# Kernel optimization log

Measured on AMD Instinct MI355X. Metric: run time of the kernel, lower is better.

## Reference

```python
import jax, jax.numpy as jnp
import numpy as np

D, H, W_IMG = 3, 128, 128
ZDIM, HDIM = 64, 512
KSEG, B = 8, 256
DIN = D * H * W_IMG


def setup_inputs() -> dict:
    key = jax.random.key(0)
    ks = jax.random.split(key, 18)
    s = 0.02
    inp = {
        "x": jax.random.normal(ks[0], (B, D, H, W_IMG), jnp.float32),
        "K": KSEG,
        "eps0": jax.random.normal(ks[1], (B, ZDIM), jnp.float32),
        "eps_q": jax.random.normal(ks[2], (KSEG - 1, B, ZDIM), jnp.float32),
        "eps_p": jax.random.normal(ks[3], (KSEG - 1, B, ZDIM), jnp.float32),
        # encoder stem (flattened image -> hdim) and gaussian head (hdim -> 2*zdim)
        "W_stem": jax.random.normal(ks[4], (DIN, HDIM), jnp.float32) * s,
        "b_stem": jnp.zeros((HDIM,), jnp.float32),
        "W_g": jax.random.normal(ks[5], (HDIM, 2 * ZDIM), jnp.float32) * s,
        "b_g": jnp.zeros((2 * ZDIM,), jnp.float32),
        # posterior LSTM (input zdim+hdim, hidden 2*zdim); initial state is always
        # zero in the original code (state is never fed back), so W_hh drops out.
        "Wih_q": jax.random.normal(ks[6], (ZDIM + HDIM, 8 * ZDIM), jnp.float32) * s,
        "b_q": jnp.zeros((8 * ZDIM,), jnp.float32),
        "Wlin_q": jax.random.normal(ks[7], (2 * ZDIM, 2 * ZDIM), jnp.float32) * s,
        "blin_q": jnp.zeros((2 * ZDIM,), jnp.float32),
        # prior LSTM (input zdim, hidden 2*zdim)
        "Wih_p": jax.random.normal(ks[8], (ZDIM, 8 * ZDIM), jnp.float32) * s,
        "b_p": jnp.zeros((8 * ZDIM,), jnp.float32),
        "Wlin_p": jax.random.normal(ks[9], (2 * ZDIM, 2 * ZDIM), jnp.float32) * s,
        "blin_p": jnp.zeros((2 * ZDIM,), jnp.float32),
        # decoder: zdim -> 1*h*w
        "W_dec": jax.random.normal(ks[10], (ZDIM, H * W_IMG), jnp.float32) * s,
        "b_dec": jnp.zeros((H * W_IMG,), jnp.float32),
    }
    return inp


def _std(logvar):
    return jax.nn.softplus(logvar + 0.5) + 1e-8


def _lstm_step_zero_state(xin, Wih, b):
    # single LSTM step with zero initial (h, c); W_hh contribution vanishes.
    g = xin @ Wih + b
    i, f, gg, o = jnp.split(g, 4, axis=-1)  # torch gate order i,f,g,o
    c = jax.nn.sigmoid(i) * jnp.tanh(gg)
    return jax.nn.sigmoid(o) * jnp.tanh(c)


def _kl_normal(mq, sq, mp, sp):
    return jnp.log(sp / sq) + (sq * sq + (mq - mp) ** 2) / (2.0 * sp * sp) - 0.5


def reference(x, K, eps0, eps_q, eps_p, W_stem, b_stem, W_g, b_g,
              Wih_q, b_q, Wlin_q, blin_q, Wih_p, b_p, Wlin_p, blin_p,
              W_dec, b_dec):
    batch = x.shape[0]
    xf = x.reshape(batch, -1)
    hf = jax.nn.relu(xf @ W_stem + b_stem)              # [B, hdim]
    enc = hf @ W_g + b_g
    mu, logvar = jnp.split(enc, 2, axis=1)
    s0 = _std(logvar)
    z0 = mu + s0 * eps0
    kl0 = -jnp.log(s0) + (s0 * s0 + mu * mu) / 2.0 - 0.5  # KL(q || N(0,1))

    def step(z_prev, eps_pair):
        eq, ep = eps_pair
        hq = _lstm_step_zero_state(jnp.concatenate([hf, z_prev], axis=1), Wih_q, b_q)
        enc_q = hq @ Wlin_q + blin_q
        mq, lq = jnp.split(enc_q, 2, axis=1)
        sq = _std(lq)
        zq = mq + sq * eq
        hp = _lstm_step_zero_state(z_prev, Wih_p, b_p)
        enc_p = hp @ Wlin_p + blin_p
        mp, lp = jnp.split(enc_p, 2, axis=1)
        sp = _std(lp)
        kl = _kl_normal(mq, sq, mp, sp)
        return zq, (zq, kl)

    _, (zq_s, kl_s) = jax.lax.scan(step, z0, (eps_q, eps_p))
    zs = jnp.concatenate([z0[None], zq_s], axis=0)       # [K, B, zdim]

    dec = (zs.reshape(K * batch, ZDIM) @ W_dec + b_dec)
    dec = dec.reshape(K, batch, 1, H, W_IMG)
    ls = jax.nn.log_sigmoid(dec)
    lns = jax.nn.log_sigmoid(-dec)
    log_ss_excl = jnp.cumsum(lns, axis=0) - lns          # exclusive prefix sum
    log_ms = log_ss_excl + ls                            # [K, B, 1, H, W]

    kl_all = jnp.concatenate([kl0[..., None], jnp.moveaxis(kl_s, 0, -1)], axis=-1)
    return log_ms, kl_all
```

## Files before the change

kernel.cpp:

```cpp
#include <hip/hip_runtime.h>
#include <hip/hip_bf16.h>

#define ZD 64
#define HD 512
#define NB 256
#define KS 8
#define DIN 49152
#define DN 16384

typedef __attribute__((ext_vector_type(8))) short bf16x8;
typedef __attribute__((ext_vector_type(4))) float f32x4;

__device__ __forceinline__ ushort bfc(float x) {
  uint u = __float_as_uint(x);
  uint r = (u + 0x7FFFu + ((u >> 16) & 1u)) >> 16;
  return (ushort)r;
}
__device__ __forceinline__ uint pk2(float a, float b) {
  return (uint)bfc(a) | ((uint)bfc(b) << 16);
}
__device__ __forceinline__ uint cvtpk(float lo, float hi) {
  uint r;
  asm("v_cvt_pk_bf16_f32 %0, %1, %2" : "=v"(r) : "v"(lo), "v"(hi));
  return r;
}
__device__ __forceinline__ float lof(uint u) { return __uint_as_float(u << 16); }
__device__ __forceinline__ float hif(uint u) { return __uint_as_float(u & 0xFFFF0000u); }
__device__ __forceinline__ float bf2f(ushort u) { return __uint_as_float((uint)u << 16); }
__device__ __forceinline__ float softplusf_(float x) {
  return fmaxf(x, 0.f) + log1pf(expf(-fabsf(x)));
}
__device__ __forceinline__ float softplus_fast(float x) {
  float e = __expf(-fabsf(x));
  return fmaxf(x, 0.f) + __logf(1.f + e);
}
__device__ __forceinline__ float sigmoidf_(float x) {
  return 1.f / (1.f + expf(-x));
}

#define SPLITS 128
#define KCH (DIN / SPLITS)
#define BKK 32

__global__ __launch_bounds__(256, 2)
void stem_prep_kernel(const float* __restrict__ x, const float* __restrict__ W,
                      ushort* __restrict__ part,
                      const float* __restrict__ Wd, ushort* __restrict__ WdT,
                      const float* __restrict__ Wihq, const float* __restrict__ Wg,
                      ushort* __restrict__ WcT, const float* __restrict__ Wihp,
                      const float* __restrict__ Wlinq, const float* __restrict__ Wlinp,
                      uint* __restrict__ wzq, uint* __restrict__ wzp,
                      uint* __restrict__ wlq, uint* __restrict__ wlp) {
  __shared__ float Af[256 * 32];
  __shared__ uint Bt[128 * 20];
  __shared__ float T[64][68];
  const int tid = threadIdx.x;

  if (blockIdx.x >= 512) {
    const int bx = blockIdx.x - 512;
    const int t = tid;
    if (bx < 64) {
      const int c = bx * 256 + t;
      uint packed[32];
#pragma unroll
      for (int k = 0; k < 32; ++k) {
        float a = Wd[(size_t)(2 * k) * DN + c];
        float b = Wd[(size_t)(2 * k + 1) * DN + c];
        packed[k] = pk2(a, b);
      }
      uint4* dst = (uint4*)&WdT[(size_t)c * 64];
#pragma unroll
      for (int i = 0; i < 8; ++i)
        dst[i] = make_uint4(packed[4 * i], packed[4 * i + 1], packed[4 * i + 2],
                            packed[4 * i + 3]);
    } else if (bx < 144) {
      const int bx2 = bx - 64;
      const int cx = bx2 % 10, ky = bx2 / 10;
      const int ct = cx * 64, kt = ky * 64;
      {
        const int rl = t >> 2, cq = (t & 3) * 16;
        const float* src = (cx < 8) ? &Wihq[(size_t)(kt + rl) * 512 + ct + cq]
                                    : &Wg[(size_t)(kt + rl) * 128 + (ct - 512) + cq];
#pragma unroll
        for (int i = 0; i < 4; ++i) {
          float4 v = *(const float4*)(src + 4 * i);
          T[rl][cq + 4 * i + 0] = v.x;
          T[rl][cq + 4 * i + 1] = v.y;
          T[rl][cq + 4 * i + 2] = v.z;
          T[rl][cq + 4 * i + 3] = v.w;
        }
      }
      __syncthreads();
      {
        const int cl = t >> 2, kq = (t & 3) * 16;
        uint* dst = (uint*)WcT;
#pragma unroll
        for (int i = 0; i < 8; ++i) {
          uint u = pk2(T[kq + 2 * i][cl], T[kq + 2 * i + 1][cl]);
          dst[(((size_t)(ct + cl)) * 512 + kt + kq + 2 * i) >> 1] = u;
        }
      }
    } else {
      const int tp = (bx - 144) * 256 + t;
#pragma unroll
      for (int r2 = 0; r2 < 4; ++r2) {
        const int i = tp * 4 + r2;
        const int zp = i >> 9, col = i & 511;
        wzq[i] = pk2(Wihq[(size_t)(HD + 2 * zp) * HD + col],
                     Wihq[(size_t)(HD + 2 * zp + 1) * HD + col]);
        wzp[i] = pk2(Wihp[(size_t)(2 * zp) * HD + col],
                     Wihp[(size_t)(2 * zp + 1) * HD + col]);
        if (i < 8192) {
          const int kp2 = i >> 7, jj = i & 127;
          wlq[i] = pk2(Wlinq[(2 * kp2) * 128 + jj], Wlinq[(2 * kp2 + 1) * 128 + jj]);
          wlp[i] = pk2(Wlinp[(2 * kp2) * 128 + jj], Wlinp[(2 * kp2 + 1) * 128 + jj]);
        }
      }
    }
    return;
  }

  const int id = blockIdx.x;
  const int nt = (id >> 3) & 3;
  const int sp = (id >> 5) * 8 + (id & 7);
  const int n0 = nt * 128;
  const int lane = tid & 63;
  const int wave = tid >> 6;
  const int wm = wave >> 1, wn = wave & 1;
  const int rr = lane & 15, gq = lane >> 4;

  f32x4 accr[8][4];
#pragma unroll
  for (int i = 0; i < 8; ++i)
#pragma unroll
    for (int j = 0; j < 4; ++j) accr[i][j] = (f32x4){0.f, 0.f, 0.f, 0.f};

  const int arow_b = tid >> 3;
  const int asub = tid & 7;
  const int bkq = tid >> 5, bn4 = tid & 31;
  auto* ldsA = (__attribute__((address_space(3))) uint*)Af;

#pragma unroll 1
  for (int it = 0; it < KCH / BKK; ++it) {
    const int k0 = sp * KCH + it * BKK;
    __syncthreads();
#pragma unroll
    for (int i = 0; i < 8; ++i) {
      const int row = i * 32 + arow_b;
      const int slot = asub ^ (row & 7);
      const float* g = x + (size_t)row * DIN + k0 + slot * 4;
      __builtin_amdgcn_global_load_lds(
          (const __attribute__((address_space(1))) uint*)g,
          ldsA + i * 1024 + wave * 256, 16, 0, 0);
    }
    {
      float4 vb[4];
#pragma unroll
      for (int j = 0; j < 4; ++j)
        vb[j] = *(const float4*)(W + (size_t)(k0 + bkq * 4 + j) * HD + n0 + bn4 * 4);
      const int gg = bkq >> 1, sb = bkq & 1;
#pragma unroll
      for (int c = 0; c < 4; ++c) {
        const int n = bn4 * 4 + c;
        const float* q0 = (const float*)&vb[0];
        const float* q1 = (const float*)&vb[1];
        const float* q2 = (const float*)&vb[2];
        const float* q3 = (const float*)&vb[3];
        uint lo = cvtpk(q0[c], q1[c]);
        uint hi = cvtpk(q2[c], q3[c]);
        const int rot = (gg + (n >> 2) + n) & 3;
        *(uint2*)&Bt[n * 20 + rot * 4 + sb * 2] = make_uint2(lo, hi);
      }
    }
    asm volatile("s_waitcnt vmcnt(0)" ::: "memory");
    __syncthreads();
    bf16x8 af[8], bfr[4];
#pragma unroll
    for (int mf = 0; mf < 8; ++mf) {
      const int r = wm * 128 + mf * 16 + rr;
      const int s = r & 7;
      float4 a0 = *(const float4*)&Af[r * 32 + ((gq * 2) ^ s) * 4];
      float4 a1 = *(const float4*)&Af[r * 32 + ((gq * 2 + 1) ^ s) * 4];
      uint4 au = make_uint4(cvtpk(a0.x, a0.y), cvtpk(a0.z, a0.w),
                            cvtpk(a1.x, a1.y), cvtpk(a1.z, a1.w));
      af[mf] = *(bf16x8*)&au;
    }
#pragma unroll
    for (int nf = 0; nf < 4; ++nf) {
      const int n = wn * 64 + nf * 16 + rr;
      const int rot = (gq + (n >> 2) + n) & 3;
      uint4 bu = *(const uint4*)&Bt[n * 20 + rot * 4];
      bfr[nf] = *(bf16x8*)&bu;
    }
#pragma unroll
    for (int mf = 0; mf < 8; ++mf)
#pragma unroll
      for (int nf = 0; nf < 4; ++nf)
        accr[mf][nf] = __builtin_amdgcn_mfma_f32_16x16x32_bf16(
            af[mf], bfr[nf], accr[mf][nf], 0, 0, 0);
  }

  const int ccol = lane & 15, crow = (lane >> 4) * 4;
  ushort* base = part + (size_t)sp * (NB * HD);
#pragma unroll
  for (int mf = 0; mf < 8; ++mf) {
#pragma unroll
    for (int nf = 0; nf < 4; ++nf) {
      const int col = n0 + wn * 64 + nf * 16 + ccol;
      const int row = wm * 128 + mf * 16 + crow;
#pragma unroll
      for (int i = 0; i < 4; ++i)
        base[(size_t)(row + i) * HD + col] = bfc(accr[mf][nf][i]);
    }
  }
}

__global__ __launch_bounds__(256)
void reduce_kernel(const ushort* __restrict__ part, float* __restrict__ acc) {
  __shared__ float4 sh[128];
  const int q4 = blockIdx.x * 128 + (threadIdx.x & 127);
  const int half = threadIdx.x >> 7;
  const ushort4* p = (const ushort4*)part;
  float4 s = {0.f, 0.f, 0.f, 0.f};
#pragma unroll 8
  for (int sp = half * 64; sp < half * 64 + 64; ++sp) {
    ushort4 v = p[(size_t)sp * (NB * HD / 4) + q4];
    s.x += bf2f(v.x); s.y += bf2f(v.y); s.z += bf2f(v.z); s.w += bf2f(v.w);
  }
  if (half) sh[threadIdx.x - 128] = s;
  __syncthreads();
  if (!half) {
    float4 o = sh[threadIdx.x];
    o.x += s.x; o.y += s.y; o.z += s.z; o.w += s.w;
    ((float4*)acc)[q4] = o;
  }
}

__global__ __launch_bounds__(256)
void gemmA_kernel(const float* __restrict__ acc, const float* __restrict__ bstem,
                  const ushort* __restrict__ WcT, const float* __restrict__ bq,
                  const float* __restrict__ bg, float* __restrict__ hfqg,
                  float* __restrict__ enc0g) {
  const int tid = threadIdx.x;
  const int lane = tid & 63;
  const int wave = tid >> 6;
  const int rr = lane & 15, gq = lane >> 4;
  const int mtile = blockIdx.y * 16;
  const int ncol = blockIdx.x * 64 + wave * 16;
  const int row = mtile + rr;

  f32x4 a4 = (f32x4){0.f, 0.f, 0.f, 0.f};
#pragma unroll
  for (int ks2 = 0; ks2 < 16; ++ks2) {
    const int k0 = ks2 * 32 + gq * 8;
    float4 x0 = *(const float4*)&acc[(size_t)row * HD + k0];
    float4 x1 = *(const float4*)&acc[(size_t)row * HD + k0 + 4];
    float4 b0 = *(const float4*)&bstem[k0];
    float4 b1 = *(const float4*)&bstem[k0 + 4];
    bf16x8 af;
    af[0] = (short)bfc(fmaxf(x0.x + b0.x, 0.f));
    af[1] = (short)bfc(fmaxf(x0.y + b0.y, 0.f));
    af[2] = (short)bfc(fmaxf(x0.z + b0.z, 0.f));
    af[3] = (short)bfc(fmaxf(x0.w + b0.w, 0.f));
    af[4] = (short)bfc(fmaxf(x1.x + b1.x, 0.f));
    af[5] = (short)bfc(fmaxf(x1.y + b1.y, 0.f));
    af[6] = (short)bfc(fmaxf(x1.z + b1.z, 0.f));
    af[7] = (short)bfc(fmaxf(x1.w + b1.w, 0.f));
    bf16x8 bf = *(const bf16x8*)&WcT[(size_t)(ncol + rr) * 512 + k0];
    a4 = __builtin_amdgcn_mfma_f32_16x16x32_bf16(af, bf, a4, 0, 0, 0);
  }
  const int col = ncol + rr;
  if (col < 512) {
    const float bb = bq[col];
#pragma unroll
    for (int i = 0; i < 4; ++i)
      hfqg[(size_t)(mtile + 4 * gq + i) * HD + col] = a4[i] + bb;
  } else {
    const float bb = bg[col - 512];
#pragma unroll
    for (int i = 0; i < 4; ++i)
      enc0g[(size_t)(mtile + 4 * gq + i) * 128 + (col - 512)] = a4[i] + bb;
  }
}

__global__ __launch_bounds__(512, 2)
void scan_kernel(const float* __restrict__ hfqg, const float* __restrict__ enc0g,
                 const uint* __restrict__ wzqg, const uint* __restrict__ wzpg,
                 const uint* __restrict__ wlqg, const uint* __restrict__ wlpg,
                 const float* __restrict__ blinq, const float* __restrict__ blinp,
                 const float* __restrict__ bp,
                 const float* __restrict__ eps0, const float* __restrict__ epsq,
                 ushort* __restrict__ zsb, float* __restrict__ out_kl) {
  const int b = blockIdx.x, tid = threadIdx.x;
  __shared__ uint WlL[2][64 * 128];
  __shared__ float g[512], gp[512];
  __shared__ float hq[128], hp[128];
  __shared__ float psum[512];
  __shared__ float zsh[64];
  __shared__ float epsL[448];

  uint wq[32], wp[32];
#pragma unroll
  for (int zp = 0; zp < 32; ++zp) {
    wq[zp] = wzqg[zp * 512 + tid];
    wp[zp] = wzpg[zp * 512 + tid];
  }
#pragma unroll
  for (int i = 0; i < 16; ++i) {
    const int idx = i * 512 + tid;
    WlL[0][idx] = wlqg[idx];
    WlL[1][idx] = wlpg[idx];
  }
  if (tid < 448) epsL[tid] = epsq[(size_t)((tid >> 6) * NB + b) * ZD + (tid & 63)];
  const float hfq_reg = hfqg[(size_t)b * HD + tid];
  const float bp_reg = bp[tid];
  if (tid < 64) {
    float mu = enc0g[b * 128 + tid], lv = enc0g[b * 128 + 64 + tid];
    float s0 = softplusf_(lv + 0.5f) + 1e-8f;
    float z0 = mu + s0 * eps0[b * ZD + tid];
    zsh[tid] = z0;
    zsb[(b * KS) * ZD + tid] = bfc(z0);
    out_kl[(b * ZD + tid) * KS] = -logf(s0) + (s0 * s0 + mu * mu) * 0.5f - 0.5f;
  }
  __syncthreads();

  for (int t = 0; t < KS - 1; ++t) {
    float aq = hfq_reg, ap = bp_reg;
#pragma unroll
    for (int zp = 0; zp < 32; ++zp) {
      float z0v = zsh[2 * zp], z1v = zsh[2 * zp + 1];
      uint uq = wq[zp], up = wp[zp];
      aq += z0v * lof(uq) + z1v * hif(uq);
      ap += z0v * lof(up) + z1v * hif(up);
    }
    g[tid] = aq;
    gp[tid] = ap;
    __syncthreads();
    if (tid < 128) {
      float cs = sigmoidf_(g[tid]) * tanhf(g[256 + tid]);
      hq[tid] = sigmoidf_(g[384 + tid]) * tanhf(cs);
    } else if (tid < 256) {
      int j = tid & 127;
      float cs = sigmoidf_(gp[j]) * tanhf(gp[256 + j]);
      hp[j] = sigmoidf_(gp[384 + j]) * tanhf(cs);
    }
    __syncthreads();
    {
      int s = tid & 255, jj = s & 127, kc = s >> 7;
      int mq_ = tid >> 8;
      const float* h = mq_ ? hp : hq;
      const uint* W = WlL[mq_];
      float a = 0.f;
#pragma unroll
      for (int kp = 0; kp < 32; ++kp) {
        uint u = W[(kc * 32 + kp) * 128 + jj];
        a += h[kc * 64 + 2 * kp] * lof(u) + h[kc * 64 + 2 * kp + 1] * hif(u);
      }
      psum[tid] = a;
    }
    __syncthreads();
    if (tid < 64) {
      float mq = psum[tid] + psum[128 + tid] + blinq[tid];
      float lq = psum[64 + tid] + psum[192 + tid] + blinq[64 + tid];
      float sq = softplusf_(lq + 0.5f) + 1e-8f;
      float zq = mq + sq * epsL[t * 64 + tid];
      float mp2 = psum[256 + tid] + psum[384 + tid] + blinp[tid];
      float lp = psum[320 + tid] + psum[448 + tid] + blinp[64 + tid];
      float sp_ = softplusf_(lp + 0.5f) + 1e-8f;
      float d = mq - mp2;
      out_kl[(b * ZD + tid) * KS + t + 1] =
          logf(sp_ / sq) + (sq * sq + d * d) / (2.f * sp_ * sp_) - 0.5f;
      zsb[(b * KS + t + 1) * ZD + tid] = bfc(zq);
      zsh[tid] = zq;
    }
    __syncthreads();
  }
}

__global__ __launch_bounds__(256)
void dec_kernel(const ushort* __restrict__ zsb, const ushort* __restrict__ WdT,
                const float* __restrict__ bd, float* __restrict__ out) {
  const int tid = threadIdx.x;
  const int lane = tid & 63;
  const int wave = tid >> 6;
  const int rr = lane & 15, gq = lane >> 4;
  const int mtile0 = blockIdx.y * 32;
  const int ncol0 = blockIdx.x * 256 + wave * 64;

  bf16x8 bfr[2][4];
#pragma unroll
  for (int ks2 = 0; ks2 < 2; ++ks2)
#pragma unroll
    for (int nf = 0; nf < 4; ++nf)
      bfr[ks2][nf] = *(const bf16x8*)&WdT[(size_t)(ncol0 + nf * 16 + rr) * 64 +
                                          ks2 * 32 + gq * 8];
  bf16x8 af[2][2];
#pragma unroll
  for (int mi = 0; mi < 2; ++mi)
#pragma unroll
    for (int ks2 = 0; ks2 < 2; ++ks2)
      af[mi][ks2] = *(const bf16x8*)&zsb[(size_t)(mtile0 + mi * 16 + rr) * 64 +
                                         ks2 * 32 + gq * 8];
  float bde[4];
#pragma unroll
  for (int nf = 0; nf < 4; ++nf) bde[nf] = bd[ncol0 + nf * 16 + rr];

  f32x4 acc[2][4];
#pragma unroll
  for (int mi = 0; mi < 2; ++mi)
#pragma unroll
    for (int nf = 0; nf < 4; ++nf) acc[mi][nf] = (f32x4){0.f, 0.f, 0.f, 0.f};

#pragma unroll
  for (int mi = 0; mi < 2; ++mi)
#pragma unroll
    for (int ks2 = 0; ks2 < 2; ++ks2)
#pragma unroll
      for (int nf = 0; nf < 4; ++nf)
        acc[mi][nf] = __builtin_amdgcn_mfma_f32_16x16x32_bf16(
            af[mi][ks2], bfr[ks2][nf], acc[mi][nf], 0, 0, 0);

  const int khi = (gq & 1) * 4;
#pragma unroll
  for (int mi = 0; mi < 2; ++mi) {
    const int bb = ((mtile0 + mi * 16) >> 3) + (gq >> 1);
#pragma unroll
    for (int nf = 0; nf < 4; ++nf) {
      const int col = ncol0 + nf * 16 + rr;
      float run = 0.f;
      float ov[4];
#pragma unroll
      for (int i = 0; i < 4; ++i) {
        float dec = acc[mi][nf][i] + bde[nf];
        float spd = softplus_fast(dec);
        ov[i] = run + (dec - spd);
        run -= spd;
      }
      float prev = __shfl_xor(run, 16, 64);
      float base = (gq & 1) ? prev : 0.f;
#pragma unroll
      for (int i = 0; i < 4; ++i)
        out[((size_t)(khi + i) * NB + bb) * DN + col] = ov[i] + base;
    }
  }
}

extern "C" void kernel_launch(void* const* d_in, const int* in_sizes, int n_in,
                              void* d_out, int out_size, void* d_ws, size_t ws_size,
                              hipStream_t stream) {
  (void)in_sizes; (void)n_in; (void)out_size; (void)ws_size;
  const float* x     = (const float*)d_in[0];
  const float* eps0  = (const float*)d_in[2];
  const float* epsq  = (const float*)d_in[3];
  const float* Wstem = (const float*)d_in[5];
  const float* bstem = (const float*)d_in[6];
  const float* Wg    = (const float*)d_in[7];
  const float* bgp   = (const float*)d_in[8];
  const float* Wihq  = (const float*)d_in[9];
  const float* bq    = (const float*)d_in[10];
  const float* Wlinq = (const float*)d_in[11];
  const float* blinq = (const float*)d_in[12];
  const float* Wihp  = (const float*)d_in[13];
  const float* bp    = (const float*)d_in[14];
  const float* Wlinp = (const float*)d_in[15];
  const float* blinp = (const float*)d_in[16];
  const float* Wd    = (const float*)d_in[17];
  const float* bd    = (const float*)d_in[18];

  float* out    = (float*)d_out;
  float* outkl  = out + (size_t)KS * NB * DN;
  float* accbuf = (float*)d_ws;
  ushort* zsb   = (ushort*)(accbuf + NB * HD);
  ushort* wdt   = zsb + (size_t)KS * NB * ZD;
  ushort* wcombT = wdt + (size_t)DN * ZD;
  float* hfqg   = (float*)(wcombT + 640 * 512);
  float* enc0g  = hfqg + NB * HD;
  uint* wzq     = (uint*)(enc0g + NB * 128);
  uint* wzp     = wzq + 32 * 512;
  uint* wlq     = wzp + 32 * 512;
  uint* wlp     = wlq + 64 * 128;
  ushort* part  = (ushort*)out;

  stem_prep_kernel<<<4 * SPLITS + 160, 256, 0, stream>>>(
      x, Wstem, part, Wd, wdt, Wihq, Wg, wcombT, Wihp, Wlinq, Wlinp,
      wzq, wzp, wlq, wlp);
  reduce_kernel<<<NB * HD / 4 / 128, 256, 0, stream>>>(part, accbuf);
  gemmA_kernel<<<dim3(10, 16), 256, 0, stream>>>(accbuf, bstem, wcombT, bq, bgp,
                                                 hfqg, enc0g);
  scan_kernel<<<NB, 512, 0, stream>>>(hfqg, enc0g, wzq, wzp, wlq, wlp,
                                      blinq, blinp, bp, eps0, epsq, zsb, outkl);
  dec_kernel<<<dim3(64, 64), 256, 0, stream>>>(zsb, wdt, bd, out);
}
```

Measured before the change: 121.5 us.

## Double-buffer stem GEMM with larger tiles and move weight prep into reduce

Restructures the split-K stem GEMM into 512-thread blocks that each cover a 256-column tile, halving the block count and the number of times the x tile is reloaded. The A and B tiles are double-buffered in LDS so global loads for the next K step are issued while the current step runs MFMAs. The weight-conversion prep blocks move out of the stem launch and into the reduce kernel so they no longer compete with the GEMM for compute units. In exchange the kernel uses more LDS and registers per block, which may reduce occupancy, and it still waits on all outstanding loads each step.

```diff
diff --git a/kernel.cpp b/kernel.cpp
--- a/kernel.cpp
+++ b/kernel.cpp
@@ -41,24 +41,141 @@
 #define SPLITS 128
 #define KCH (DIN / SPLITS)
 #define BKK 32
-
-__global__ __launch_bounds__(256, 2)
-void stem_prep_kernel(const float* __restrict__ x, const float* __restrict__ W,
-                      ushort* __restrict__ part,
-                      const float* __restrict__ Wd, ushort* __restrict__ WdT,
-                      const float* __restrict__ Wihq, const float* __restrict__ Wg,
-                      ushort* __restrict__ WcT, const float* __restrict__ Wihp,
-                      const float* __restrict__ Wlinq, const float* __restrict__ Wlinp,
-                      uint* __restrict__ wzq, uint* __restrict__ wzp,
-                      uint* __restrict__ wlq, uint* __restrict__ wlp) {
-  __shared__ float Af[256 * 32];
-  __shared__ uint Bt[128 * 20];
+#define NSTEP (KCH / BKK)
+
+__global__ __launch_bounds__(512, 2)
+void stem_kernel(const float* __restrict__ x, const float* __restrict__ W,
+                 ushort* __restrict__ part) {
+  __shared__ float Af[2 * 8192];
+  __shared__ uint Bt[2 * 5120];
+  const int id = blockIdx.x;
+  const int nt = (id >> 3) & 1;
+  const int sp = (id >> 4) * 8 + (id & 7);
+  const int n0 = nt * 256;
+  const int tid = threadIdx.x;
+  const int lane = tid & 63;
+  const int wave = tid >> 6;
+  const int wm = wave >> 1, wn = wave & 1;
+  const int rr = lane & 15, gq = lane >> 4;
+
+  f32x4 accr[4][8];
+#pragma unroll
+  for (int i = 0; i < 4; ++i)
+#pragma unroll
+    for (int j = 0; j < 8; ++j) accr[i][j] = (f32x4){0.f, 0.f, 0.f, 0.f};
+
+  const int bkq = tid >> 6, bn4 = tid & 63;
+  auto* ldsA = (__attribute__((address_space(3))) uint*)Af;
+  float4 rB[4];
+
+  auto gloadA = [&](int k0, int p) {
+#pragma unroll
+    for (int i = 0; i < 4; ++i) {
+      const int row = i * 64 + (tid >> 3);
+      const int slot = (tid & 7) ^ (row & 7);
+      const float* g = x + (size_t)row * DIN + k0 + slot * 4;
+      __builtin_amdgcn_global_load_lds(
+          (const __attribute__((address_space(1))) uint*)g,
+          ldsA + p * 8192 + i * 2048 + wave * 256, 16, 0, 0);
+    }
+  };
+  auto loadB = [&](int k0) {
+#pragma unroll
+    for (int j = 0; j < 4; ++j)
+      rB[j] = *(const float4*)(W + (size_t)(k0 + bkq * 4 + j) * HD + n0 + bn4 * 4);
+  };
+  auto writeB = [&](int p) {
+    const int gg = bkq >> 1, sb = bkq & 1;
+    const float* q = (const float*)rB;
+#pragma unroll
+    for (int c = 0; c < 4; ++c) {
+      const int n = bn4 * 4 + c;
+      uint lo = cvtpk(q[0 * 4 + c], q[1 * 4 + c]);
+      uint hi = cvtpk(q[2 * 4 + c], q[3 * 4 + c]);
+      const int rot = (gg + (n >> 2) + n) & 3;
+      *(uint2*)&Bt[p * 5120 + n * 20 + rot * 4 + sb * 2] = make_uint2(lo, hi);
+    }
+  };
+  auto compute = [&](int p) {
+    bf16x8 af[4], bfr[8];
+#pragma unroll
+    for (int mf = 0; mf < 4; ++mf) {
+      const int r = wm * 64 + mf * 16 + rr;
+      const int s = r & 7;
+      float4 a0 = *(const float4*)&Af[p * 8192 + r * 32 + ((gq * 2) ^ s) * 4];
+      float4 a1 = *(const float4*)&Af[p * 8192 + r * 32 + ((gq * 2 + 1) ^ s) * 4];
+      uint4 au = make_uint4(cvtpk(a0.x, a0.y), cvtpk(a0.z, a0.w),
+                            cvtpk(a1.x, a1.y), cvtpk(a1.z, a1.w));
+      af[mf] = *(bf16x8*)&au;
+    }
+#pragma unroll
+    for (int nf = 0; nf < 8; ++nf) {
+      const int n = wn * 128 + nf * 16 + rr;
+      const int rot = (gq + (n >> 2) + n) & 3;
+      uint4 bu = *(const uint4*)&Bt[p * 5120 + n * 20 + rot * 4];
+      bfr[nf] = *(bf16x8*)&bu;
+    }
+#pragma unroll
+    for (int mf = 0; mf < 4; ++mf)
+#pragma unroll
+      for (int nf = 0; nf < 8; ++nf)
+        accr[mf][nf] = __builtin_amdgcn_mfma_f32_16x16x32_bf16(
+            af[mf], bfr[nf], accr[mf][nf], 0, 0, 0);
+  };
+
+  const int kb = sp * KCH;
+  gloadA(kb, 0);
+  loadB(kb);
+  asm volatile("s_waitcnt vmcnt(0)" ::: "memory");
+  writeB(0);
+  gloadA(kb + BKK, 1);
+  loadB(kb + BKK);
+  __syncthreads();
+
+#pragma unroll 1
+  for (int t = 0; t < NSTEP; ++t) {
+    compute(t & 1);
+    if (t < NSTEP - 1) {
+      asm volatile("s_waitcnt vmcnt(0)" ::: "memory");
+      __syncthreads();
+      writeB((t + 1) & 1);
+      if (t < NSTEP - 2) {
+        gloadA(kb + (t + 2) * BKK, t & 1);
+        loadB(kb + (t + 2) * BKK);
+      }
+      __syncthreads();
+    }
+  }
+
+  const int ccol = lane & 15, crow = (lane >> 4) * 4;
+  ushort* base = part + (size_t)sp * (NB * HD);
+#pragma unroll
+  for (int mf = 0; mf < 4; ++mf) {
+#pragma unroll
+    for (int nf = 0; nf < 8; ++nf) {
+      const int col = n0 + wn * 128 + nf * 16 + ccol;
+      const int row = wm * 64 + mf * 16 + crow;
+#pragma unroll
+      for (int i = 0; i < 4; ++i)
+        base[(size_t)(row + i) * HD + col] = bfc(accr[mf][nf][i]);
+    }
+  }
+}
+
+__global__ __launch_bounds__(256)
+void reduce_prep_kernel(const ushort* __restrict__ part, float* __restrict__ acc,
+                        const float* __restrict__ Wd, ushort* __restrict__ WdT,
+                        const float* __restrict__ Wihq, const float* __restrict__ Wg,
+                        ushort* __restrict__ WcT, const float* __restrict__ Wihp,
+                        const float* __restrict__ Wlinq, const float* __restrict__ Wlinp,
+                        uint* __restrict__ wzq, uint* __restrict__ wzp,
+                        uint* __restrict__ wlq, uint* __restrict__ wlp) {
+  __shared__ float4 sh[128];
   __shared__ float T[64][68];
-  const int tid = threadIdx.x;
-
-  if (blockIdx.x >= 512) {
-    const int bx = blockIdx.x - 512;
-    const int t = tid;
+  const int t = threadIdx.x;
+
+  if (blockIdx.x >= 256) {
+    const int bx = blockIdx.x - 256;
     if (bx < 64) {
       const int c = bx * 256 + t;
       uint packed[32];
@@ -120,106 +237,8 @@
     return;
   }
 
-  const int id = blockIdx.x;
-  const int nt = (id >> 3) & 3;
-  const int sp = (id >> 5) * 8 + (id & 7);
-  const int n0 = nt * 128;
-  const int lane = tid & 63;
-  const int wave = tid >> 6;
-  const int wm = wave >> 1, wn = wave & 1;
-  const int rr = lane & 15, gq = lane >> 4;
-
-  f32x4 accr[8][4];
-#pragma unroll
-  for (int i = 0; i < 8; ++i)
-#pragma unroll
-    for (int j = 0; j < 4; ++j) accr[i][j] = (f32x4){0.f, 0.f, 0.f, 0.f};
-
-  const int arow_b = tid >> 3;
-  const int asub = tid & 7;
-  const int bkq = tid >> 5, bn4 = tid & 31;
-  auto* ldsA = (__attribute__((address_space(3))) uint*)Af;
-
-#pragma unroll 1
-  for (int it = 0; it < KCH / BKK; ++it) {
-    const int k0 = sp * KCH + it * BKK;
-    __syncthreads();
-#pragma unroll
-    for (int i = 0; i < 8; ++i) {
-      const int row = i * 32 + arow_b;
-      const int slot = asub ^ (row & 7);
-      const float* g = x + (size_t)row * DIN + k0 + slot * 4;
-      __builtin_amdgcn_global_load_lds(
-          (const __attribute__((address_space(1))) uint*)g,
-          ldsA + i * 1024 + wave * 256, 16, 0, 0);
-    }
-    {
-      float4 vb[4];
-#pragma unroll
-      for (int j = 0; j < 4; ++j)
-        vb[j] = *(const float4*)(W + (size_t)(k0 + bkq * 4 + j) * HD + n0 + bn4 * 4);
-      const int gg = bkq >> 1, sb = bkq & 1;
-#pragma unroll
-      for (int c = 0; c < 4; ++c) {
-        const int n = bn4 * 4 + c;
-        const float* q0 = (const float*)&vb[0];
-        const float* q1 = (const float*)&vb[1];
-        const float* q2 = (const float*)&vb[2];
-        const float* q3 = (const float*)&vb[3];
-        uint lo = cvtpk(q0[c], q1[c]);
-        uint hi = cvtpk(q2[c], q3[c]);
-        const int rot = (gg + (n >> 2) + n) & 3;
-        *(uint2*)&Bt[n * 20 + rot * 4 + sb * 2] = make_uint2(lo, hi);
-      }
-    }
-    asm volatile("s_waitcnt vmcnt(0)" ::: "memory");
-    __syncthreads();
-    bf16x8 af[8], bfr[4];
-#pragma unroll
-    for (int mf = 0; mf < 8; ++mf) {
-      const int r = wm * 128 + mf * 16 + rr;
-      const int s = r & 7;
-      float4 a0 = *(const float4*)&Af[r * 32 + ((gq * 2) ^ s) * 4];
-      float4 a1 = *(const float4*)&Af[r * 32 + ((gq * 2 + 1) ^ s) * 4];
-      uint4 au = make_uint4(cvtpk(a0.x, a0.y), cvtpk(a0.z, a0.w),
-                            cvtpk(a1.x, a1.y), cvtpk(a1.z, a1.w));
-      af[mf] = *(bf16x8*)&au;
-    }
-#pragma unroll
-    for (int nf = 0; nf < 4; ++nf) {
-      const int n = wn * 64 + nf * 16 + rr;
-      const int rot = (gq + (n >> 2) + n) & 3;
-      uint4 bu = *(const uint4*)&Bt[n * 20 + rot * 4];
-      bfr[nf] = *(bf16x8*)&bu;
-    }
-#pragma unroll
-    for (int mf = 0; mf < 8; ++mf)
-#pragma unroll
-      for (int nf = 0; nf < 4; ++nf)
-        accr[mf][nf] = __builtin_amdgcn_mfma_f32_16x16x32_bf16(
-            af[mf], bfr[nf], accr[mf][nf], 0, 0, 0);
-  }
-
-  const int ccol = lane & 15, crow = (lane >> 4) * 4;
-  ushort* base = part + (size_t)sp * (NB * HD);
-#pragma unroll
-  for (int mf = 0; mf < 8; ++mf) {
-#pragma unroll
-    for (int nf = 0; nf < 4; ++nf) {
-      const int col = n0 + wn * 64 + nf * 16 + ccol;
-      const int row = wm * 128 + mf * 16 + crow;
-#pragma unroll
-      for (int i = 0; i < 4; ++i)
-        base[(size_t)(row + i) * HD + col] = bfc(accr[mf][nf][i]);
-    }
-  }
-}
-
-__global__ __launch_bounds__(256)
-void reduce_kernel(const ushort* __restrict__ part, float* __restrict__ acc) {
-  __shared__ float4 sh[128];
-  const int q4 = blockIdx.x * 128 + (threadIdx.x & 127);
-  const int half = threadIdx.x >> 7;
+  const int q4 = blockIdx.x * 128 + (t & 127);
+  const int half = t >> 7;
   const ushort4* p = (const ushort4*)part;
   float4 s = {0.f, 0.f, 0.f, 0.f};
 #pragma unroll 8
@@ -227,10 +246,10 @@
     ushort4 v = p[(size_t)sp * (NB * HD / 4) + q4];
     s.x += bf2f(v.x); s.y += bf2f(v.y); s.z += bf2f(v.z); s.w += bf2f(v.w);
   }
-  if (half) sh[threadIdx.x - 128] = s;
+  if (half) sh[t - 128] = s;
   __syncthreads();
   if (!half) {
-    float4 o = sh[threadIdx.x];
+    float4 o = sh[t];
     o.x += s.x; o.y += s.y; o.z += s.z; o.w += s.w;
     ((float4*)acc)[q4] = o;
   }
@@ -481,10 +500,10 @@
   uint* wlp     = wlq + 64 * 128;
   ushort* part  = (ushort*)out;
 
-  stem_prep_kernel<<<4 * SPLITS + 160, 256, 0, stream>>>(
-      x, Wstem, part, Wd, wdt, Wihq, Wg, wcombT, Wihp, Wlinq, Wlinp,
-      wzq, wzp, wlq, wlp);
-  reduce_kernel<<<NB * HD / 4 / 128, 256, 0, stream>>>(part, accbuf);
+  stem_kernel<<<256, 512, 0, stream>>>(x, Wstem, part);
+  reduce_prep_kernel<<<416, 256, 0, stream>>>(part, accbuf, Wd, wdt, Wihq, Wg,
+                                              wcombT, Wihp, Wlinq, Wlinp,
+                                              wzq, wzp, wlq, wlp);
   gemmA_kernel<<<dim3(10, 16), 256, 0, stream>>>(accbuf, bstem, wcombT, bq, bgp,
                                                  hfqg, enc0g);
   scan_kernel<<<NB, 512, 0, stream>>>(hfqg, enc0g, wzq, wzp, wlq, wlp,
```

Result: slower. 128.0 us (+5.4%).

## Pre-convert input images to bf16 in a separate pass before the stem GEMM

Applied to the files above, without the earlier changes.

Adds a conversion pass that writes x as bf16 into scratch space inside the output buffer. The stem GEMM then loads bf16 A tiles directly into LDS and feeds them to the MFMA without per-iteration cvt instructions. Each stem block's A traffic is halved because it reads bf16, and the weight-prep work moves into the conversion kernel. The cost is an extra launch plus a full read of x (48MB fp32) and write of 24MB bf16 before the GEMM. This may cost more than it saves, since x is read four times in the GEMM (once per N-tile).

```diff
diff --git a/kernel.cpp b/kernel.cpp
--- a/kernel.cpp
+++ b/kernel.cpp
@@ -38,92 +38,99 @@
   return 1.f / (1.f + expf(-x));
 }
 
-#define SPLITS 128
-#define KCH (DIN / SPLITS)
-#define BKK 32
-
-__global__ __launch_bounds__(256, 2)
-void stem_prep_kernel(const float* __restrict__ x, const float* __restrict__ W,
-                      ushort* __restrict__ part,
+__global__ __launch_bounds__(256)
+void conv_prep_kernel(const float* __restrict__ x, ushort* __restrict__ xb,
                       const float* __restrict__ Wd, ushort* __restrict__ WdT,
                       const float* __restrict__ Wihq, const float* __restrict__ Wg,
                       ushort* __restrict__ WcT, const float* __restrict__ Wihp,
                       const float* __restrict__ Wlinq, const float* __restrict__ Wlinp,
                       uint* __restrict__ wzq, uint* __restrict__ wzp,
                       uint* __restrict__ wlq, uint* __restrict__ wlp) {
-  __shared__ float Af[256 * 32];
+  __shared__ float T[64][68];
+  const int t = threadIdx.x;
+  if (blockIdx.x < 6144) {
+    const size_t i0 = ((size_t)blockIdx.x * 256 + t) * 8;
+    float4 v0 = *(const float4*)&x[i0];
+    float4 v1 = *(const float4*)&x[i0 + 4];
+    *(uint4*)&xb[i0] = make_uint4(pk2(v0.x, v0.y), pk2(v0.z, v0.w),
+                                  pk2(v1.x, v1.y), pk2(v1.z, v1.w));
+    return;
+  }
+  const int bx = blockIdx.x - 6144;
+  if (bx < 64) {
+    const int c = bx * 256 + t;
+    uint packed[32];
+#pragma unroll
+    for (int k = 0; k < 32; ++k) {
+      float a = Wd[(size_t)(2 * k) * DN + c];
+      float b = Wd[(size_t)(2 * k + 1) * DN + c];
+      packed[k] = pk2(a, b);
+    }
+    uint4* dst = (uint4*)&WdT[(size_t)c * 64];
+#pragma unroll
+    for (int i = 0; i < 8; ++i)
+      dst[i] = make_uint4(packed[4 * i], packed[4 * i + 1], packed[4 * i + 2],
+                          packed[4 * i + 3]);
+  } else if (bx < 144) {
+    const int bx2 = bx - 64;
+    const int cx = bx2 % 10, ky = bx2 / 10;
+    const int ct = cx * 64, kt = ky * 64;
+    {
+      const int rl = t >> 2, cq = (t & 3) * 16;
+      const float* src = (cx < 8) ? &Wihq[(size_t)(kt + rl) * 512 + ct + cq]
+                                  : &Wg[(size_t)(kt + rl) * 128 + (ct - 512) + cq];
+#pragma unroll
+      for (int i = 0; i < 4; ++i) {
+        float4 v = *(const float4*)(src + 4 * i);
+        T[rl][cq + 4 * i + 0] = v.x;
+        T[rl][cq + 4 * i + 1] = v.y;
+        T[rl][cq + 4 * i + 2] = v.z;
+        T[rl][cq + 4 * i + 3] = v.w;
+      }
+    }
+    __syncthreads();
+    {
+      const int cl = t >> 2, kq = (t & 3) * 16;
+      uint* dst = (uint*)WcT;
+#pragma unroll
+      for (int i = 0; i < 8; ++i) {
+        uint u = pk2(T[kq + 2 * i][cl], T[kq + 2 * i + 1][cl]);
+        dst[(((size_t)(ct + cl)) * 512 + kt + kq + 2 * i) >> 1] = u;
+      }
+    }
+  } else {
+    const int tp = (bx - 144) * 256 + t;
+#pragma unroll
+    for (int r2 = 0; r2 < 4; ++r2) {
+      const int i = tp * 4 + r2;
+      const int zp = i >> 9, col = i & 511;
+      wzq[i] = pk2(Wihq[(size_t)(HD + 2 * zp) * HD + col],
+                   Wihq[(size_t)(HD + 2 * zp + 1) * HD + col]);
+      wzp[i] = pk2(Wihp[(size_t)(2 * zp) * HD + col],
+                   Wihp[(size_t)(2 * zp + 1) * HD + col]);
+      if (i < 8192) {
+        const int kp2 = i >> 7, jj = i & 127;
+        wlq[i] = pk2(Wlinq[(2 * kp2) * 128 + jj], Wlinq[(2 * kp2 + 1) * 128 + jj]);
+        wlp[i] = pk2(Wlinp[(2 * kp2) * 128 + jj], Wlinp[(2 * kp2 + 1) * 128 + jj]);
+      }
+    }
+  }
+}
+
+#define SPLITS 128
+#define KCH (DIN / SPLITS)
+#define BKK 32
+
+__global__ __launch_bounds__(256, 2)
+void stem_kernel(const ushort* __restrict__ xb, const float* __restrict__ W,
+                 ushort* __restrict__ part) {
+  __shared__ ushort Ab[256 * 32];
   __shared__ uint Bt[128 * 20];
-  __shared__ float T[64][68];
-  const int tid = threadIdx.x;
-
-  if (blockIdx.x >= 512) {
-    const int bx = blockIdx.x - 512;
-    const int t = tid;
-    if (bx < 64) {
-      const int c = bx * 256 + t;
-      uint packed[32];
-#pragma unroll
-      for (int k = 0; k < 32; ++k) {
-        float a = Wd[(size_t)(2 * k) * DN + c];
-        float b = Wd[(size_t)(2 * k + 1) * DN + c];
-        packed[k] = pk2(a, b);
-      }
-      uint4* dst = (uint4*)&WdT[(size_t)c * 64];
-#pragma unroll
-      for (int i = 0; i < 8; ++i)
-        dst[i] = make_uint4(packed[4 * i], packed[4 * i + 1], packed[4 * i + 2],
-                            packed[4 * i + 3]);
-    } else if (bx < 144) {
-      const int bx2 = bx - 64;
-      const int cx = bx2 % 10, ky = bx2 / 10;
-      const int ct = cx * 64, kt = ky * 64;
-      {
-        const int rl = t >> 2, cq = (t & 3) * 16;
-        const float* src = (cx < 8) ? &Wihq[(size_t)(kt + rl) * 512 + ct + cq]
-                                    : &Wg[(size_t)(kt + rl) * 128 + (ct - 512) + cq];
-#pragma unroll
-        for (int i = 0; i < 4; ++i) {
-          float4 v = *(const float4*)(src + 4 * i);
-          T[rl][cq + 4 * i + 0] = v.x;
-          T[rl][cq + 4 * i + 1] = v.y;
-          T[rl][cq + 4 * i + 2] = v.z;
-          T[rl][cq + 4 * i + 3] = v.w;
-        }
-      }
-      __syncthreads();
-      {
-        const int cl = t >> 2, kq = (t & 3) * 16;
-        uint* dst = (uint*)WcT;
-#pragma unroll
-        for (int i = 0; i < 8; ++i) {
-          uint u = pk2(T[kq + 2 * i][cl], T[kq + 2 * i + 1][cl]);
-          dst[(((size_t)(ct + cl)) * 512 + kt + kq + 2 * i) >> 1] = u;
-        }
-      }
-    } else {
-      const int tp = (bx - 144) * 256 + t;
-#pragma unroll
-      for (int r2 = 0; r2 < 4; ++r2) {
-        const int i = tp * 4 + r2;
-        const int zp = i >> 9, col = i & 511;
-        wzq[i] = pk2(Wihq[(size_t)(HD + 2 * zp) * HD + col],
-                     Wihq[(size_t)(HD + 2 * zp + 1) * HD + col]);
-        wzp[i] = pk2(Wihp[(size_t)(2 * zp) * HD + col],
-                     Wihp[(size_t)(2 * zp + 1) * HD + col]);
-        if (i < 8192) {
-          const int kp2 = i >> 7, jj = i & 127;
-          wlq[i] = pk2(Wlinq[(2 * kp2) * 128 + jj], Wlinq[(2 * kp2 + 1) * 128 + jj]);
-          wlp[i] = pk2(Wlinp[(2 * kp2) * 128 + jj], Wlinp[(2 * kp2 + 1) * 128 + jj]);
-        }
-      }
-    }
-    return;
-  }
-
   const int id = blockIdx.x;
   const int nt = (id >> 3) & 3;
   const int sp = (id >> 5) * 8 + (id & 7);
   const int n0 = nt * 128;
+  const int tid = threadIdx.x;
   const int lane = tid & 63;
   const int wave = tid >> 6;
   const int wm = wave >> 1, wn = wave & 1;
@@ -135,20 +142,20 @@
 #pragma unroll
     for (int j = 0; j < 4; ++j) accr[i][j] = (f32x4){0.f, 0.f, 0.f, 0.f};
 
-  const int arow_b = tid >> 3;
-  const int asub = tid & 7;
+  const int arow_b = tid >> 2;
+  const int aslot = tid & 3;
   const int bkq = tid >> 5, bn4 = tid & 31;
-  auto* ldsA = (__attribute__((address_space(3))) uint*)Af;
+  auto* ldsA = (__attribute__((address_space(3))) uint*)Ab;
 
 #pragma unroll 1
   for (int it = 0; it < KCH / BKK; ++it) {
     const int k0 = sp * KCH + it * BKK;
     __syncthreads();
 #pragma unroll
-    for (int i = 0; i < 8; ++i) {
-      const int row = i * 32 + arow_b;
-      const int slot = asub ^ (row & 7);
-      const float* g = x + (size_t)row * DIN + k0 + slot * 4;
+    for (int i = 0; i < 4; ++i) {
+      const int row = i * 64 + arow_b;
+      const int slot = aslot ^ (row & 3);
+      const ushort* g = xb + (size_t)row * DIN + k0 + slot * 8;
       __builtin_amdgcn_global_load_lds(
           (const __attribute__((address_space(1))) uint*)g,
           ldsA + i * 1024 + wave * 256, 16, 0, 0);
@@ -178,12 +185,8 @@
 #pragma unroll
     for (int mf = 0; mf < 8; ++mf) {
       const int r = wm * 128 + mf * 16 + rr;
-      const int s = r & 7;
-      float4 a0 = *(const float4*)&Af[r * 32 + ((gq * 2) ^ s) * 4];
-      float4 a1 = *(const float4*)&Af[r * 32 + ((gq * 2 + 1) ^ s) * 4];
-      uint4 au = make_uint4(cvtpk(a0.x, a0.y), cvtpk(a0.z, a0.w),
-                            cvtpk(a1.x, a1.y), cvtpk(a1.z, a1.w));
-      af[mf] = *(bf16x8*)&au;
+      const int g = gq ^ (r & 3);
+      af[mf] = *(const bf16x8*)&Ab[r * 32 + g * 8];
     }
 #pragma unroll
     for (int nf = 0; nf < 4; ++nf) {
@@ -480,10 +483,11 @@
   uint* wlq     = wzp + 32 * 512;
   uint* wlp     = wlq + 64 * 128;
   ushort* part  = (ushort*)out;
-
-  stem_prep_kernel<<<4 * SPLITS + 160, 256, 0, stream>>>(
-      x, Wstem, part, Wd, wdt, Wihq, Wg, wcombT, Wihp, Wlinq, Wlinp,
-      wzq, wzp, wlq, wlp);
+  ushort* xbuf  = part + (size_t)SPLITS * NB * HD;
+
+  conv_prep_kernel<<<6144 + 160, 256, 0, stream>>>(
+      x, xbuf, Wd, wdt, Wihq, Wg, wcombT, Wihp, Wlinq, Wlinp, wzq, wzp, wlq, wlp);
+  stem_kernel<<<4 * SPLITS, 256, 0, stream>>>(xbuf, Wstem, part);
   reduce_kernel<<<NB * HD / 4 / 128, 256, 0, stream>>>(part, accbuf);
   gemmA_kernel<<<dim3(10, 16), 256, 0, stream>>>(accbuf, bstem, wcombT, bq, bgp,
                                                  hfqg, enc0g);
```

Measured after the change: 142.1 us. +17.0%, slower.
